# Optimization experiments

Hardware: AMD Instinct MI355X
Metric: run time of the kernel (lower is better)

The kernel has to match this reference:

```python
import jax, jax.numpy as jnp
import numpy as np

B, L, D, C, H, NB = 2, 2048, 256, 8, 8, 2
S = 2                        # spatial coord dim of s
E = 2 * D - (C + 1)          # id-embedding width per D*2-(C+1)
FIN = 1 + S + E + C          # z + s + id-embed + conditionals
MAXLOC = 4096
DH = (2 * D) // H            # per-head dim


def _ln(x, sc, b):
    m = x.mean(-1, keepdims=True)
    v = ((x - m) ** 2).mean(-1, keepdims=True)
    return (x - m) * jax.lax.rsqrt(v + 1e-6) * sc + b


def setup_inputs() -> dict:
    key = jax.random.key(0)
    ks = iter(jax.random.split(key, 64))
    nrm = lambda shape: jax.random.normal(next(ks), shape, jnp.float32) * 0.02
    inp = {
        "z": jax.random.normal(next(ks), (B, L), jnp.float32),
        "conditionals": jax.random.normal(next(ks), (C,), jnp.float32),
        "s": jax.random.uniform(next(ks), (L, S), jnp.float32),
        "K": jax.random.uniform(next(ks), (L, L), jnp.float32),
        "embed": nrm((MAXLOC, E)),
        "W_in1": nrm((FIN, 4 * D)), "b_in1": jnp.zeros((4 * D,), jnp.float32),
        "W_in2": nrm((4 * D, D)), "b_in2": jnp.zeros((D,), jnp.float32),
        "bias_w": jnp.ones((NB,), jnp.float32), "bias_b": jnp.zeros((NB,), jnp.float32),
        "Wq": nrm((NB, D, 2 * D)), "bq": jnp.zeros((NB, 2 * D), jnp.float32),
        "Wk": nrm((NB, D, 2 * D)), "bk": jnp.zeros((NB, 2 * D), jnp.float32),
        "Wv": nrm((NB, D, 2 * D)), "bv": jnp.zeros((NB, 2 * D), jnp.float32),
        "Wo": nrm((NB, 2 * D, D)), "bo": jnp.zeros((NB, D), jnp.float32),
        "ln1_s": jnp.ones((NB, D), jnp.float32), "ln1_b": jnp.zeros((NB, D), jnp.float32),
        "ln2_s": jnp.ones((NB, D), jnp.float32), "ln2_b": jnp.zeros((NB, D), jnp.float32),
        "Wf1": nrm((NB, D, 4 * D)), "bf1": jnp.zeros((NB, 4 * D), jnp.float32),
        "Wf2": nrm((NB, 4 * D, D)), "bf2": jnp.zeros((NB, D), jnp.float32),
        "Wh1": nrm((D, 128)), "bh1": jnp.zeros((128,), jnp.float32),
        "Wh2": nrm((128, 1)), "bh2": jnp.zeros((1,), jnp.float32),
    }
    return inp


def reference(z, conditionals, s, K, embed, W_in1, b_in1, W_in2, b_in2,
              bias_w, bias_b, Wq, bq, Wk, bk, Wv, bv, Wo, bo,
              ln1_s, ln1_b, ln2_s, ln2_b, Wf1, bf1, Wf2, bf2,
              Wh1, bh1, Wh2, bh2):
    Bx, Lx = z.shape
    ids_e = embed[:Lx]  # ids = arange(L), so embedding lookup is a leading slice
    feats = jnp.concatenate([
        z[..., None],                                          # (B, L, 1)
        jnp.broadcast_to(s[None], (Bx, Lx, S)),                # (B, L, S)
        jnp.broadcast_to(ids_e[None], (Bx, Lx, E)),            # (B, L, E)
        jnp.broadcast_to(conditionals[None, None], (Bx, Lx, C)),  # cond_as_feats
    ], axis=-1)
    x = jax.nn.gelu(feats @ W_in1 + b_in1) @ W_in2 + b_in2     # (B, L, D)
    for i in range(NB):
        bias = bias_w[i] * K + bias_b[i]                        # learned scalar-affine kernel bias (L, L)
        h = _ln(x, ln1_s[i], ln1_b[i])
        q = (h @ Wq[i] + bq[i]).reshape(Bx, Lx, H, DH)
        k = (h @ Wk[i] + bk[i]).reshape(Bx, Lx, H, DH)
        v = (h @ Wv[i] + bv[i]).reshape(Bx, Lx, H, DH)
        scores = jnp.einsum('bqhd,bkhd->bhqk', q, k) / jnp.sqrt(jnp.float32(DH))
        scores = scores + bias[None, None]                      # broadcast over batch, heads
        a = jax.nn.softmax(scores, axis=-1)
        o = jnp.einsum('bhqk,bkhd->bqhd', a, v).reshape(Bx, Lx, 2 * D)
        x = x + (o @ Wo[i] + bo[i])
        h2 = _ln(x, ln2_s[i], ln2_b[i])
        x = x + jax.nn.gelu(h2 @ Wf1[i] + bf1[i]) @ Wf2[i] + bf2[i]
    return jax.nn.gelu(x @ Wh1 + bh1) @ Wh2 + bh2              # head MLP([128,1]) -> (B, L, 1)
```

## Files before the change

kernel.cpp:

```cpp
#include <hip/hip_runtime.h>
#include <math.h>

#define B_SZ 2
#define L_LEN 2048
#define D_MOD 256
#define H_HEADS 8
#define NB_BLK 2
#define S_SZ 2
#define E_SZ 503
#define C_SZ 8
#define FIN 514
#define FIN_PAD 576
#define LOG2E 1.44269504088896340736f
#define QSC (0.125f * LOG2E)

typedef short bf16x8 __attribute__((ext_vector_type(8)));
typedef float f32x4 __attribute__((ext_vector_type(4)));
typedef unsigned short u16x4 __attribute__((ext_vector_type(4)));
typedef unsigned short u16x8 __attribute__((ext_vector_type(8)));

#define OFF_IN1 0
#define OFF_IN2 589824
#define OFF_QKV 851968
#define OFF_O   1638400
#define OFF_F1  1900544
#define OFF_F2  2424832
#define OFF_H   2949120
#define WT_END  2981888

__device__ __forceinline__ unsigned short f2bf(float x) {
    unsigned u = __float_as_uint(x);
    u += 0x7FFFu + ((u >> 16) & 1u);
    return (unsigned short)(u >> 16);
}

__device__ __forceinline__ float gelu_f(float x) {
    float x3 = x * x * x;
    return 0.5f * x * (1.0f + tanhf(0.7978845608028654f * (x + 0.044715f * x3)));
}

__device__ __forceinline__ void gll16(const void* g, void* l) {
    __builtin_amdgcn_global_load_lds(
        (const __attribute__((address_space(1))) unsigned int*)g,
        (__attribute__((address_space(3))) unsigned int*)l,
        16, 0, 0);
}

__global__ __launch_bounds__(256) void feats_kernel(
    const float* __restrict__ z, const float* __restrict__ s,
    const float* __restrict__ embed, const float* __restrict__ cond,
    unsigned short* __restrict__ feats)
{
    int idx = blockIdx.x * 256 + threadIdx.x;
    const int total = B_SZ * L_LEN * FIN_PAD;
    if (idx >= total) return;
    int f = idx % FIN_PAD;
    int row = idx / FIN_PAD;
    int l = row % L_LEN;
    float val;
    if (f == 0)                   val = z[row];
    else if (f < 1 + S_SZ)        val = s[l * S_SZ + (f - 1)];
    else if (f < 1 + S_SZ + E_SZ) val = embed[(size_t)l * E_SZ + (f - 3)];
    else if (f < FIN)             val = cond[f - (1 + S_SZ + E_SZ)];
    else                          val = 0.0f;
    feats[idx] = f2bf(val);
}

__global__ __launch_bounds__(256) void wprep_kernel(
    const float* __restrict__ W_in1, const float* __restrict__ W_in2,
    const float* __restrict__ Wq, const float* __restrict__ Wk,
    const float* __restrict__ Wv, const float* __restrict__ Wo,
    const float* __restrict__ Wf1, const float* __restrict__ Wf2,
    const float* __restrict__ Wh1, unsigned short* __restrict__ wt)
{
    int b = blockIdx.x;
    const float* src; unsigned short* dst; int K, N, Kp, tile;
    float scale = 1.0f;
    if (b < 144)      { src = W_in1; dst = wt + OFF_IN1; K = 514;  N = 1024; Kp = 576;  tile = b; }
    else if (b < 208) { src = W_in2; dst = wt + OFF_IN2; K = 1024; N = 256;  Kp = 1024; tile = b - 144; }
    else if (b < 400) { int t2 = b - 208;
                        int sec = t2 >> 5; tile = t2 & 31;
                        int i = sec / 3, which = sec % 3;
                        const float* wsrc = which == 0 ? Wq : which == 1 ? Wk : Wv;
                        if (which == 0) scale = QSC;
                        src = wsrc + (size_t)i * 131072;
                        dst = wt + OFF_QKV + (size_t)i * 393216 + (size_t)which * 131072;
                        K = 256; N = 512; Kp = 256; }
    else if (b < 464) { int t2 = b - 400; int i = t2 >> 5; tile = t2 & 31;
                        src = Wo + (size_t)i * 131072; dst = wt + OFF_O + (size_t)i * 131072;
                        K = 512; N = 256; Kp = 512; }
    else if (b < 592) { int t2 = b - 464; int i = t2 >> 6; tile = t2 & 63;
                        src = Wf1 + (size_t)i * 262144; dst = wt + OFF_F1 + (size_t)i * 262144;
                        K = 256; N = 1024; Kp = 256; }
    else if (b < 720) { int t2 = b - 592; int i = t2 >> 6; tile = t2 & 63;
                        src = Wf2 + (size_t)i * 262144; dst = wt + OFF_F2 + (size_t)i * 262144;
                        K = 1024; N = 256; Kp = 1024; }
    else              { tile = b - 720; src = Wh1; dst = wt + OFF_H;
                        K = 256; N = 128; Kp = 256; }

    int nt = N >> 6;
    int kt0 = (tile / nt) << 6;
    int nt0 = (tile % nt) << 6;

    __shared__ unsigned short sT[64][65];
    int t = threadIdx.x;
    #pragma unroll
    for (int p = 0; p < 4; p++) {
        int r = p * 16 + (t >> 4);
        int c = (t & 15) * 4;
        float4 v4 = make_float4(0.f, 0.f, 0.f, 0.f);
        if (kt0 + r < K) v4 = *(const float4*)(src + (size_t)(kt0 + r) * N + nt0 + c);
        sT[r][c + 0] = f2bf(v4.x * scale);
        sT[r][c + 1] = f2bf(v4.y * scale);
        sT[r][c + 2] = f2bf(v4.z * scale);
        sT[r][c + 3] = f2bf(v4.w * scale);
    }
    __syncthreads();
    int n = t >> 2, kq = (t & 3) * 16;
    u16x8 o0, o1;
    #pragma unroll
    for (int j = 0; j < 8; j++) {
        o0[j] = sT[kq + j][n];
        o1[j] = sT[kq + 8 + j][n];
    }
    unsigned short* dp = dst + (size_t)(nt0 + n) * Kp + kt0 + kq;
    *(u16x8*)(dp) = o0;
    *(u16x8*)(dp + 8) = o1;
}

__global__ __launch_bounds__(256) void kprep_kernel(
    const float* __restrict__ Kmat, const float* __restrict__ bias_w,
    unsigned short* __restrict__ kbt)
{
    __shared__ float sT[64][65];
    int tile = blockIdx.x;
    int qt0 = (tile & 31) << 6, kt0 = (tile >> 5) << 6;
    int t = threadIdx.x;
    int rr = t >> 4, cc = (t & 15) << 2;
    #pragma unroll
    for (int p = 0; p < 4; p++) {
        int qr = p * 16 + rr;
        float4 v4 = *(const float4*)(Kmat + (size_t)(qt0 + qr) * L_LEN + kt0 + cc);
        sT[cc + 0][qr] = v4.x;
        sT[cc + 1][qr] = v4.y;
        sT[cc + 2][qr] = v4.z;
        sT[cc + 3][qr] = v4.w;
    }
    __syncthreads();
    float s0 = bias_w[0] * LOG2E, s1 = bias_w[1] * LOG2E;
    int kr = t >> 2, qc = (t & 3) << 4;
    u16x8 a0, a1, b0, b1;
    #pragma unroll
    for (int j = 0; j < 8; j++) {
        float v = sT[kr][qc + j];
        a0[j] = f2bf(v * s0); b0[j] = f2bf(v * s1);
        float v2 = sT[kr][qc + 8 + j];
        a1[j] = f2bf(v2 * s0); b1[j] = f2bf(v2 * s1);
    }
    unsigned short* d0 = kbt + (size_t)(kt0 + kr) * L_LEN + qt0 + qc;
    *(u16x8*)d0 = a0; *(u16x8*)(d0 + 8) = a1;
    unsigned short* d1 = d0 + (size_t)L_LEN * L_LEN;
    *(u16x8*)d1 = b0; *(u16x8*)(d1 + 8) = b1;
}

__global__ __launch_bounds__(256) void bprep_kernel(
    const float* __restrict__ bq, const float* __restrict__ bk,
    const float* __restrict__ bv, float* __restrict__ bqkv)
{
    int idx = blockIdx.x * 256 + threadIdx.x;
    if (idx >= 2 * 1536) return;
    int i = idx / 1536, c = idx % 1536;
    float v;
    if (c < 512)       v = bq[i * 512 + c] * QSC;
    else if (c < 1024) v = bk[i * 512 + c - 512];
    else               v = bv[i * 512 + c - 1024];
    bqkv[idx] = v;
}

__global__ __launch_bounds__(256) void cvt_kernel(
    const float* __restrict__ x, unsigned short* __restrict__ xb)
{
    int idx = (blockIdx.x * 256 + threadIdx.x) * 8;
    float4 a = *(const float4*)(x + idx);
    float4 b = *(const float4*)(x + idx + 4);
    u16x8 o = { f2bf(a.x), f2bf(a.y), f2bf(a.z), f2bf(a.w),
                f2bf(b.x), f2bf(b.y), f2bf(b.z), f2bf(b.w) };
    *(u16x8*)(xb + idx) = o;
}

template<int ACT, int OMODE, int BM>
__global__ __launch_bounds__(256) void gemm_bf16(
    const unsigned short* __restrict__ A, const unsigned short* __restrict__ Wt,
    const float* __restrict__ bias, float* __restrict__ Cf,
    unsigned short* __restrict__ Cb, unsigned short* __restrict__ Cbk,
    unsigned short* __restrict__ Cbv, int M, int N, int Kd, int lda)
{
    __shared__ unsigned short sA[2][BM][64];
    __shared__ unsigned short sB[2][64][64];
    const int tid = threadIdx.x;
    const int l = tid & 63, w = tid >> 6;
    const int g = l >> 4, n16 = l & 15;
    const int m0 = blockIdx.y * BM, n0 = blockIdx.x * 64;

    const int r8 = l >> 3;
    const int swz8 = ((l & 7) ^ r8) * 8;

    const int NMI = (BM == 64) ? 2 : 1;
    const int wr = (BM == 64) ? (w >> 1) : (w >> 1);
    const int wc = w & 1;

    f32x4 acc[2][2];
    #pragma unroll
    for (int mi = 0; mi < 2; mi++)
        #pragma unroll
        for (int ni = 0; ni < 2; ni++)
            acc[mi][ni] = (f32x4){0.f, 0.f, 0.f, 0.f};

#define STAGE(buf, k0)                                                          \
    do {                                                                        \
        if (BM == 64) {                                                         \
            _Pragma("unroll")                                                   \
            for (int p = 0; p < 2; p++) {                                       \
                int row = w * 16 + p * 8 + r8;                                  \
                gll16(A + (size_t)(m0 + row) * lda + (k0) + swz8,               \
                      &sA[buf][w * 16 + p * 8][0]);                             \
            }                                                                   \
        } else {                                                                \
            int row = w * 8 + r8;                                               \
            gll16(A + (size_t)(m0 + row) * lda + (k0) + swz8,                   \
                  &sA[buf][w * 8][0]);                                          \
        }                                                                       \
        _Pragma("unroll")                                                       \
        for (int p = 0; p < 2; p++) {                                           \
            int row = w * 16 + p * 8 + r8;                                      \
            gll16(Wt + (size_t)(n0 + row) * Kd + (k0) + swz8,                   \
                  &sB[buf][w * 16 + p * 8][0]);                                 \
        }                                                                       \
    } while (0)

    STAGE(0, 0);
    __syncthreads();

    int cur = 0;
    for (int k0 = 0; k0 < Kd; k0 += 64) {
        int nxt = cur ^ 1;
        if (k0 + 64 < Kd) STAGE(nxt, k0 + 64);
        #pragma unroll
        for (int ks = 0; ks < 2; ks++) {
            bf16x8 af[2], bfr[2];
            #pragma unroll
            for (int mi = 0; mi < NMI; mi++) {
                int row = (BM == 64) ? (wr * 32 + mi * 16 + n16) : (wr * 16 + n16);
                af[mi] = *(const bf16x8*)((const char*)&sA[cur][row][0]
                          + ((ks * 64 + g * 16) ^ ((n16 & 7) << 4)));
            }
            #pragma unroll
            for (int ni = 0; ni < 2; ni++) {
                int row = wc * 32 + ni * 16 + n16;
                bfr[ni] = *(const bf16x8*)((const char*)&sB[cur][row][0]
                          + ((ks * 64 + g * 16) ^ ((n16 & 7) << 4)));
            }
            #pragma unroll
            for (int mi = 0; mi < NMI; mi++)
                #pragma unroll
                for (int ni = 0; ni < 2; ni++)
                    acc[mi][ni] = __builtin_amdgcn_mfma_f32_16x16x32_bf16(
                        af[mi], bfr[ni], acc[mi][ni], 0, 0, 0);
        }
        __syncthreads();
        cur = nxt;
    }
#undef STAGE

    #pragma unroll
    for (int mi = 0; mi < NMI; mi++) {
        #pragma unroll
        for (int ni = 0; ni < 2; ni++) {
            int col = n0 + wc * 32 + ni * 16 + n16;
            float bv = bias[col];
            #pragma unroll
            for (int r = 0; r < 4; r++) {
                int row = (BM == 64) ? (m0 + wr * 32 + mi * 16 + 4 * g + r)
                                     : (m0 + wr * 16 + 4 * g + r);
                float val = acc[mi][ni][r] + bv;
                if (ACT == 1) val = gelu_f(val);
                if (OMODE == 0) {
                    Cf[(size_t)row * N + col] = val;
                } else if (OMODE == 1) {
                    Cb[(size_t)row * N + col] = f2bf(val);
                } else if (OMODE == 2) {
                    float* cp = Cf + (size_t)row * N + col;
                    *cp += val;
                } else {
                    if (col < 1024) {
                        unsigned short* dst = (col < 512) ? Cb : Cbk;
                        dst[(size_t)row * 512 + (col & 511)] = f2bf(val);
                    } else {
                        Cbv[((size_t)(row >> 11) * 512 + (col - 1024)) * L_LEN + (row & (L_LEN - 1))] = f2bf(val);
                    }
                }
            }
        }
    }
}

__global__ __launch_bounds__(256) void ln_bf16(
    const float* __restrict__ x, const float* __restrict__ sc,
    const float* __restrict__ bi, unsigned short* __restrict__ out)
{
    int wave = threadIdx.x >> 6, lane = threadIdx.x & 63;
    int row = blockIdx.x * 4 + wave;
    const float* xr = x + (size_t)row * D_MOD;
    float4 v = *(const float4*)(xr + lane * 4);
    float s1 = v.x + v.y + v.z + v.w;
    float s2 = v.x * v.x + v.y * v.y + v.z * v.z + v.w * v.w;
    #pragma unroll
    for (int off = 1; off < 64; off <<= 1) {
        s1 += __shfl_xor(s1, off);
        s2 += __shfl_xor(s2, off);
    }
    float mean = s1 * (1.0f / 256.0f);
    float var = s2 * (1.0f / 256.0f) - mean * mean;
    float rs = rsqrtf(var + 1e-6f);
    float4 scv = *(const float4*)(sc + lane * 4);
    float4 bv  = *(const float4*)(bi + lane * 4);
    u16x4 o4;
    o4[0] = f2bf((v.x - mean) * rs * scv.x + bv.x);
    o4[1] = f2bf((v.y - mean) * rs * scv.y + bv.y);
    o4[2] = f2bf((v.z - mean) * rs * scv.z + bv.z);
    o4[3] = f2bf((v.w - mean) * rs * scv.w + bv.w);
    *(u16x4*)(out + (size_t)row * D_MOD + lane * 4) = o4;
}

__global__ __launch_bounds__(256, 3) void attn_mfma(
    const unsigned short* __restrict__ q, const unsigned short* __restrict__ k,
    const unsigned short* __restrict__ vt, const unsigned short* __restrict__ kmt,
    unsigned short* __restrict__ o)
{
    __shared__ unsigned short sK[2][64][64];
    __shared__ unsigned short sV[2][64][64];
    __shared__ unsigned short sKmT[64][64];
    __shared__ unsigned short sP[4][16][72];

    const int tid = threadIdx.x;
    const int l = tid & 63, w = tid >> 6;
    const int g = l >> 4, n16 = l & 15;
    const int qblk = blockIdx.x * 64, hh = blockIdx.y, b = blockIdx.z;

    const int r8 = l >> 3;
    const int swz8 = ((l & 7) ^ r8) * 8;

    bf16x8 qf[2];
    {
        const unsigned short* qp = q + (size_t)(b * L_LEN + qblk + w * 16 + n16) * 512 + hh * 64;
        qf[0] = *(const bf16x8*)(qp + g * 8);
        qf[1] = *(const bf16x8*)(qp + 32 + g * 8);
    }
    bf16x8 onesf;
    #pragma unroll
    for (int j = 0; j < 8; j++) onesf[j] = (short)0x3F80;

    f32x4 o_acc[4];
    #pragma unroll
    for (int c = 0; c < 4; c++) o_acc[c] = (f32x4){0.f, 0.f, 0.f, 0.f};
    f32x4 l_acc = (f32x4){0.f, 0.f, 0.f, 0.f};

    const unsigned short* kbase = k + (size_t)b * L_LEN * 512 + hh * 64;
    const unsigned short* vbase = vt + ((size_t)b * 512 + hh * 64) * L_LEN;

    #pragma unroll
    for (int p = 0; p < 2; p++) {
        int row = w * 16 + p * 8 + r8;
        gll16(kbase + (size_t)row * 512 + swz8, &sK[0][w * 16 + p * 8][0]);
        gll16(vbase + (size_t)row * L_LEN + swz8, &sV[0][w * 16 + p * 8][0]);
        gll16(kmt + (size_t)row * L_LEN + qblk + swz8, &sKmT[w * 16 + p * 8][0]);
    }
    __syncthreads();

    int cur = 0;
    for (int kt = 0; kt < L_LEN / 64; kt++) {
        const int nb = cur ^ 1;
        const int kblk2 = (kt + 1) << 6;
        if (kt + 1 < L_LEN / 64) {
            #pragma unroll
            for (int p = 0; p < 2; p++) {
                int row = w * 16 + p * 8 + r8;
                gll16(kbase + (size_t)(kblk2 + row) * 512 + swz8, &sK[nb][w * 16 + p * 8][0]);
                gll16(vbase + (size_t)row * L_LEN + kblk2 + swz8, &sV[nb][w * 16 + p * 8][0]);
            }
        }
        f32x4 sacc[4];
        #pragma unroll
        for (int c = 0; c < 4; c++) {
            const char* kb_ = (const char*)&sKmT[c * 16 + n16][0];
            u16x4 kmv = *(const u16x4*)(kb_ + ((32 * w + 8 * g) ^ ((n16 & 7) << 4)));
            #pragma unroll
            for (int r = 0; r < 4; r++)
                sacc[c][r] = __uint_as_float(((unsigned)(unsigned short)kmv[r]) << 16);
        }
        #pragma unroll
        for (int ks = 0; ks < 2; ks++)
            #pragma unroll
            for (int c = 0; c < 4; c++) {
                int row = c * 16 + n16;
                bf16x8 kf = *(const bf16x8*)((const char*)&sK[cur][row][0]
                             + ((ks * 64 + g * 16) ^ ((n16 & 7) << 4)));
                sacc[c] = __builtin_amdgcn_mfma_f32_16x16x32_bf16(qf[ks], kf, sacc[c], 0, 0, 0);
            }
        float p[4][4];
        #pragma unroll
        for (int r = 0; r < 4; r++)
            #pragma unroll
            for (int c = 0; c < 4; c++)
                p[r][c] = __builtin_amdgcn_exp2f(sacc[c][r]);
        asm volatile("s_waitcnt lgkmcnt(0)" ::: "memory");
        __builtin_amdgcn_s_barrier();
        __builtin_amdgcn_sched_barrier(0);
        if (kt + 1 < L_LEN / 64) {
            #pragma unroll
            for (int p2 = 0; p2 < 2; p2++) {
                int row = w * 16 + p2 * 8 + r8;
                gll16(kmt + (size_t)(kblk2 + row) * L_LEN + qblk + swz8,
                      &sKmT[w * 16 + p2 * 8][0]);
            }
        }
        #pragma unroll
        for (int r = 0; r < 4; r++)
            #pragma unroll
            for (int c = 0; c < 4; c++)
                sP[w][4 * g + r][c * 16 + n16] = f2bf(p[r][c]);
        #pragma unroll
        for (int ks = 0; ks < 2; ks++) {
            bf16x8 pf = *(const bf16x8*)&sP[w][n16][ks * 32 + g * 8];
            l_acc = __builtin_amdgcn_mfma_f32_16x16x32_bf16(pf, onesf, l_acc, 0, 0, 0);
            #pragma unroll
            for (int c = 0; c < 4; c++) {
                int row = c * 16 + n16;
                bf16x8 vf = *(const bf16x8*)((const char*)&sV[cur][row][0]
                             + ((ks * 64 + g * 16) ^ ((n16 & 7) << 4)));
                o_acc[c] = __builtin_amdgcn_mfma_f32_16x16x32_bf16(pf, vf, o_acc[c], 0, 0, 0);
            }
        }
        __syncthreads();
        cur = nb;
    }

    float inv[4];
    #pragma unroll
    for (int r = 0; r < 4; r++) inv[r] = 1.0f / l_acc[r];
    #pragma unroll
    for (int c = 0; c < 4; c++)
        #pragma unroll
        for (int r = 0; r < 4; r++)
            o[(size_t)(b * L_LEN + qblk + w * 16 + 4 * g + r) * 512 + hh * 64 + c * 16 + n16]
                = f2bf(o_acc[c][r] * inv[r]);
}

__global__ __launch_bounds__(256) void hsum_kernel(
    const unsigned short* __restrict__ hb, const float* __restrict__ Wh2,
    const float* __restrict__ bh2, float* __restrict__ out)
{
    int wave = threadIdx.x >> 6, lane = threadIdx.x & 63;
    int row = blockIdx.x * 4 + wave;
    unsigned v = *(const unsigned*)(hb + (size_t)row * 128 + lane * 2);
    float v0 = __uint_as_float((v & 0xFFFFu) << 16);
    float v1 = __uint_as_float(v & 0xFFFF0000u);
    float val = v0 * Wh2[lane * 2] + v1 * Wh2[lane * 2 + 1];
    #pragma unroll
    for (int off = 1; off < 64; off <<= 1)
        val += __shfl_xor(val, off);
    if (lane == 0) out[row] = val + bh2[0];
}

extern "C" void kernel_launch(void* const* d_in, const int* in_sizes, int n_in,
                              void* d_out, int out_size, void* d_ws, size_t ws_size,
                              hipStream_t stream)
{
    const float* z      = (const float*)d_in[0];
    const float* cond   = (const float*)d_in[1];
    const float* s      = (const float*)d_in[2];
    const float* Kmat   = (const float*)d_in[3];
    const float* embed  = (const float*)d_in[4];
    const float* W_in1  = (const float*)d_in[5];
    const float* b_in1  = (const float*)d_in[6];
    const float* W_in2  = (const float*)d_in[7];
    const float* b_in2  = (const float*)d_in[8];
    const float* bias_w = (const float*)d_in[9];
    const float* bias_b = (const float*)d_in[10];
    const float* Wq     = (const float*)d_in[11];
    const float* bq     = (const float*)d_in[12];
    const float* Wk     = (const float*)d_in[13];
    const float* bk     = (const float*)d_in[14];
    const float* Wv     = (const float*)d_in[15];
    const float* bv     = (const float*)d_in[16];
    const float* Wo     = (const float*)d_in[17];
    const float* bo     = (const float*)d_in[18];
    const float* ln1_s  = (const float*)d_in[19];
    const float* ln1_b  = (const float*)d_in[20];
    const float* ln2_s  = (const float*)d_in[21];
    const float* ln2_b  = (const float*)d_in[22];
    const float* Wf1    = (const float*)d_in[23];
    const float* bf1    = (const float*)d_in[24];
    const float* Wf2    = (const float*)d_in[25];
    const float* bf2    = (const float*)d_in[26];
    const float* Wh1    = (const float*)d_in[27];
    const float* bh1    = (const float*)d_in[28];
    const float* Wh2    = (const float*)d_in[29];
    const float* bh2    = (const float*)d_in[30];
    float* out = (float*)d_out;
    (void)bias_b;

    const int M = B_SZ * L_LEN;
    char* base = (char*)d_ws;
    unsigned short* feats = (unsigned short*)base;
    float* x = (float*)(base + (size_t)M * FIN_PAD * 2);
    unsigned short* h    = (unsigned short*)((char*)x + (size_t)M * D_MOD * 4);
    unsigned short* hid1 = h    + (size_t)M * D_MOD;
    unsigned short* qb   = hid1 + (size_t)M * 1024;
    unsigned short* kb2  = qb   + (size_t)M * 512;
    unsigned short* vtb  = kb2  + (size_t)M * 512;
    unsigned short* ob   = vtb  + (size_t)M * 512;
    unsigned short* wt   = ob   + (size_t)M * 512;
    float* bqkv          = (float*)(wt + WT_END);
    unsigned short* kbt  = (unsigned short*)(bqkv + 2 * 1536);

    wprep_kernel<<<dim3(728), dim3(256), 0, stream>>>(W_in1, W_in2, Wq, Wk, Wv, Wo, Wf1, Wf2, Wh1, wt);
    kprep_kernel<<<dim3(1024), dim3(256), 0, stream>>>(Kmat, bias_w, kbt);
    bprep_kernel<<<dim3(12), dim3(256), 0, stream>>>(bq, bk, bv, bqkv);
    feats_kernel<<<dim3((M * FIN_PAD) / 256), dim3(256), 0, stream>>>(z, s, embed, cond, feats);

    gemm_bf16<1, 1, 64><<<dim3(16, 64), 256, 0, stream>>>(feats, wt + OFF_IN1, b_in1, nullptr, hid1, nullptr, nullptr, M, 1024, FIN_PAD, FIN_PAD);
    gemm_bf16<0, 0, 32><<<dim3(4, 128), 256, 0, stream>>>(hid1, wt + OFF_IN2, b_in2, x, nullptr, nullptr, nullptr, M, 256, 1024, 1024);

    for (int i = 0; i < NB_BLK; i++) {
        ln_bf16<<<dim3(M / 4), 256, 0, stream>>>(x, ln1_s + i * D_MOD, ln1_b + i * D_MOD, h);
        gemm_bf16<0, 4, 64><<<dim3(24, 64), 256, 0, stream>>>(h, wt + OFF_QKV + (size_t)i * 393216, bqkv + i * 1536, nullptr, qb, kb2, vtb, M, 1536, 256, 256);
        attn_mfma<<<dim3(L_LEN / 64, H_HEADS, B_SZ), 256, 0, stream>>>(qb, kb2, vtb, kbt + (size_t)i * L_LEN * L_LEN, ob);
        gemm_bf16<0, 2, 32><<<dim3(4, 128), 256, 0, stream>>>(ob, wt + OFF_O + (size_t)i * 131072, bo + i * D_MOD, x, nullptr, nullptr, nullptr, M, 256, 512, 512);
        ln_bf16<<<dim3(M / 4), 256, 0, stream>>>(x, ln2_s + i * D_MOD, ln2_b + i * D_MOD, h);
        gemm_bf16<1, 1, 64><<<dim3(16, 64), 256, 0, stream>>>(h, wt + OFF_F1 + (size_t)i * 262144, bf1 + i * 1024, nullptr, hid1, nullptr, nullptr, M, 1024, 256, 256);
        gemm_bf16<0, 2, 32><<<dim3(4, 128), 256, 0, stream>>>(hid1, wt + OFF_F2 + (size_t)i * 262144, bf2 + i * D_MOD, x, nullptr, nullptr, nullptr, M, 256, 1024, 1024);
    }
    cvt_kernel<<<dim3(512), dim3(256), 0, stream>>>(x, h);
    gemm_bf16<1, 1, 64><<<dim3(2, 64), 256, 0, stream>>>(h, wt + OFF_H, bh1, nullptr, qb, nullptr, nullptr, M, 128, 256, 256);
    hsum_kernel<<<dim3(M / 4), 256, 0, stream>>>(qb, Wh2, bh2, out);
}
```

Baseline: 258.0 us.

## Split attention over KV halves, load kernel bias into registers, split-bf16 head GEMM

```diff
diff --git a/kernel.cpp b/kernel.cpp
--- a/kernel.cpp
+++ b/kernel.cpp
@@ -26,12 +26,16 @@
 #define OFF_F1  1900544
 #define OFF_F2  2424832
 #define OFF_H   2949120
-#define WT_END  2981888
+#define WT_END  3047424
 
 __device__ __forceinline__ unsigned short f2bf(float x) {
     unsigned u = __float_as_uint(x);
     u += 0x7FFFu + ((u >> 16) & 1u);
     return (unsigned short)(u >> 16);
+}
+
+__device__ __forceinline__ float bf2f(unsigned short h) {
+    return __uint_as_float(((unsigned)h) << 16);
 }
 
 __device__ __forceinline__ float gelu_f(float x) {
@@ -71,7 +75,7 @@
     const float* __restrict__ Wq, const float* __restrict__ Wk,
     const float* __restrict__ Wv, const float* __restrict__ Wo,
     const float* __restrict__ Wf1, const float* __restrict__ Wf2,
-    const float* __restrict__ Wh1, unsigned short* __restrict__ wt)
+    unsigned short* __restrict__ wt)
 {
     int b = blockIdx.x;
     const float* src; unsigned short* dst; int K, N, Kp, tile;
@@ -92,11 +96,9 @@
     else if (b < 592) { int t2 = b - 464; int i = t2 >> 6; tile = t2 & 63;
                         src = Wf1 + (size_t)i * 262144; dst = wt + OFF_F1 + (size_t)i * 262144;
                         K = 256; N = 1024; Kp = 256; }
-    else if (b < 720) { int t2 = b - 592; int i = t2 >> 6; tile = t2 & 63;
+    else              { int t2 = b - 592; int i = t2 >> 6; tile = t2 & 63;
                         src = Wf2 + (size_t)i * 262144; dst = wt + OFF_F2 + (size_t)i * 262144;
                         K = 1024; N = 256; Kp = 1024; }
-    else              { tile = b - 720; src = Wh1; dst = wt + OFF_H;
-                        K = 256; N = 128; Kp = 256; }
 
     int nt = N >> 6;
     int kt0 = (tile / nt) << 6;
@@ -128,6 +130,19 @@
     *(u16x8*)(dp + 8) = o1;
 }
 
+__global__ __launch_bounds__(256) void hprep_kernel(
+    const float* __restrict__ Wh1, unsigned short* __restrict__ whb)
+{
+    int idx = blockIdx.x * 256 + threadIdx.x;
+    if (idx >= 128 * 768) return;
+    int n = idx / 768, kk = idx % 768;
+    int kz = kk & 255;
+    float v = Wh1[(size_t)kz * 128 + n];
+    unsigned short hi = f2bf(v);
+    unsigned short res = (kk < 512) ? hi : f2bf(v - bf2f(hi));
+    whb[idx] = res;
+}
+
 __global__ __launch_bounds__(256) void kprep_kernel(
     const float* __restrict__ Kmat, const float* __restrict__ bias_w,
     unsigned short* __restrict__ kbt)
@@ -177,15 +192,24 @@
     bqkv[idx] = v;
 }
 
-__global__ __launch_bounds__(256) void cvt_kernel(
+__global__ __launch_bounds__(256) void xsplit_kernel(
     const float* __restrict__ x, unsigned short* __restrict__ xb)
 {
-    int idx = (blockIdx.x * 256 + threadIdx.x) * 8;
-    float4 a = *(const float4*)(x + idx);
-    float4 b = *(const float4*)(x + idx + 4);
-    u16x8 o = { f2bf(a.x), f2bf(a.y), f2bf(a.z), f2bf(a.w),
-                f2bf(b.x), f2bf(b.y), f2bf(b.z), f2bf(b.w) };
-    *(u16x8*)(xb + idx) = o;
+    int t = blockIdx.x * 256 + threadIdx.x;
+    int row = t >> 5, c8 = (t & 31) * 8;
+    const float* xr = x + (size_t)row * 256 + c8;
+    float4 a = *(const float4*)(xr);
+    float4 b4 = *(const float4*)(xr + 4);
+    u16x8 hi = { f2bf(a.x), f2bf(a.y), f2bf(a.z), f2bf(a.w),
+                 f2bf(b4.x), f2bf(b4.y), f2bf(b4.z), f2bf(b4.w) };
+    u16x8 lo = { f2bf(a.x - bf2f(hi[0])), f2bf(a.y - bf2f(hi[1])),
+                 f2bf(a.z - bf2f(hi[2])), f2bf(a.w - bf2f(hi[3])),
+                 f2bf(b4.x - bf2f(hi[4])), f2bf(b4.y - bf2f(hi[5])),
+                 f2bf(b4.z - bf2f(hi[6])), f2bf(b4.w - bf2f(hi[7])) };
+    unsigned short* orow = xb + (size_t)row * 768;
+    *(u16x8*)(orow + c8) = hi;
+    *(u16x8*)(orow + 256 + c8) = lo;
+    *(u16x8*)(orow + 512 + c8) = hi;
 }
 
 template<int ACT, int OMODE, int BM>
@@ -206,7 +230,7 @@
     const int swz8 = ((l & 7) ^ r8) * 8;
 
     const int NMI = (BM == 64) ? 2 : 1;
-    const int wr = (BM == 64) ? (w >> 1) : (w >> 1);
+    const int wr = w >> 1;
     const int wc = w & 1;
 
     f32x4 acc[2][2];
@@ -335,17 +359,18 @@
 __global__ __launch_bounds__(256, 3) void attn_mfma(
     const unsigned short* __restrict__ q, const unsigned short* __restrict__ k,
     const unsigned short* __restrict__ vt, const unsigned short* __restrict__ kmt,
-    unsigned short* __restrict__ o)
+    float* __restrict__ po, float* __restrict__ pl)
 {
     __shared__ unsigned short sK[2][64][64];
     __shared__ unsigned short sV[2][64][64];
-    __shared__ unsigned short sKmT[64][64];
     __shared__ unsigned short sP[4][16][72];
 
     const int tid = threadIdx.x;
     const int l = tid & 63, w = tid >> 6;
     const int g = l >> 4, n16 = l & 15;
-    const int qblk = blockIdx.x * 64, hh = blockIdx.y, b = blockIdx.z;
+    const int qblk = blockIdx.x * 64, hh = blockIdx.y;
+    const int b = blockIdx.z >> 1, part = blockIdx.z & 1;
+    const int kv0 = part * 1024;
 
     const int r8 = l >> 3;
     const int swz8 = ((l & 7) ^ r8) * 8;
@@ -365,39 +390,45 @@
     for (int c = 0; c < 4; c++) o_acc[c] = (f32x4){0.f, 0.f, 0.f, 0.f};
     f32x4 l_acc = (f32x4){0.f, 0.f, 0.f, 0.f};
 
-    const unsigned short* kbase = k + (size_t)b * L_LEN * 512 + hh * 64;
-    const unsigned short* vbase = vt + ((size_t)b * 512 + hh * 64) * L_LEN;
+    const unsigned short* kbase = k + ((size_t)(b * L_LEN) + kv0) * 512 + hh * 64;
+    const unsigned short* vbase = vt + ((size_t)b * 512 + hh * 64) * L_LEN + kv0;
+    const unsigned short* kmbase = kmt + (size_t)kv0 * L_LEN + qblk + 16 * w + 4 * g;
+
+    u16x4 kmC[4], kmN[4];
 
     #pragma unroll
     for (int p = 0; p < 2; p++) {
         int row = w * 16 + p * 8 + r8;
         gll16(kbase + (size_t)row * 512 + swz8, &sK[0][w * 16 + p * 8][0]);
         gll16(vbase + (size_t)row * L_LEN + swz8, &sV[0][w * 16 + p * 8][0]);
-        gll16(kmt + (size_t)row * L_LEN + qblk + swz8, &sKmT[w * 16 + p * 8][0]);
-    }
+    }
+    #pragma unroll
+    for (int c = 0; c < 4; c++)
+        kmC[c] = *(const u16x4*)(kmbase + (size_t)(c * 16 + n16) * L_LEN);
     __syncthreads();
 
     int cur = 0;
-    for (int kt = 0; kt < L_LEN / 64; kt++) {
+    for (int kt = 0; kt < 16; kt++) {
         const int nb = cur ^ 1;
         const int kblk2 = (kt + 1) << 6;
-        if (kt + 1 < L_LEN / 64) {
+        if (kt + 1 < 16) {
             #pragma unroll
             for (int p = 0; p < 2; p++) {
                 int row = w * 16 + p * 8 + r8;
                 gll16(kbase + (size_t)(kblk2 + row) * 512 + swz8, &sK[nb][w * 16 + p * 8][0]);
                 gll16(vbase + (size_t)row * L_LEN + kblk2 + swz8, &sV[nb][w * 16 + p * 8][0]);
             }
+            #pragma unroll
+            for (int c = 0; c < 4; c++)
+                kmN[c] = *(const u16x4*)(kmbase + (size_t)(kblk2 + c * 16 + n16) * L_LEN);
         }
         f32x4 sacc[4];
         #pragma unroll
-        for (int c = 0; c < 4; c++) {
-            const char* kb_ = (const char*)&sKmT[c * 16 + n16][0];
-            u16x4 kmv = *(const u16x4*)(kb_ + ((32 * w + 8 * g) ^ ((n16 & 7) << 4)));
+        for (int c = 0; c < 4; c++)
             #pragma unroll
             for (int r = 0; r < 4; r++)
-                sacc[c][r] = __uint_as_float(((unsigned)(unsigned short)kmv[r]) << 16);
-        }
+                sacc[c][r] = bf2f((unsigned short)kmC[c][r]);
+        __builtin_amdgcn_s_setprio(1);
         #pragma unroll
         for (int ks = 0; ks < 2; ks++)
             #pragma unroll
@@ -407,28 +438,19 @@
                              + ((ks * 64 + g * 16) ^ ((n16 & 7) << 4)));
                 sacc[c] = __builtin_amdgcn_mfma_f32_16x16x32_bf16(qf[ks], kf, sacc[c], 0, 0, 0);
             }
+        __builtin_amdgcn_s_setprio(0);
         float p[4][4];
         #pragma unroll
         for (int r = 0; r < 4; r++)
             #pragma unroll
             for (int c = 0; c < 4; c++)
                 p[r][c] = __builtin_amdgcn_exp2f(sacc[c][r]);
-        asm volatile("s_waitcnt lgkmcnt(0)" ::: "memory");
-        __builtin_amdgcn_s_barrier();
-        __builtin_amdgcn_sched_barrier(0);
-        if (kt + 1 < L_LEN / 64) {
-            #pragma unroll
-            for (int p2 = 0; p2 < 2; p2++) {
-                int row = w * 16 + p2 * 8 + r8;
-                gll16(kmt + (size_t)(kblk2 + row) * L_LEN + qblk + swz8,
-                      &sKmT[w * 16 + p2 * 8][0]);
-            }
-        }
         #pragma unroll
         for (int r = 0; r < 4; r++)
             #pragma unroll
             for (int c = 0; c < 4; c++)
                 sP[w][4 * g + r][c * 16 + n16] = f2bf(p[r][c]);
+        __builtin_amdgcn_s_setprio(1);
         #pragma unroll
         for (int ks = 0; ks < 2; ks++) {
             bf16x8 pf = *(const bf16x8*)&sP[w][n16][ks * 32 + g * 8];
@@ -441,19 +463,42 @@
                 o_acc[c] = __builtin_amdgcn_mfma_f32_16x16x32_bf16(pf, vf, o_acc[c], 0, 0, 0);
             }
         }
+        __builtin_amdgcn_s_setprio(0);
         __syncthreads();
         cur = nb;
-    }
-
-    float inv[4];
-    #pragma unroll
-    for (int r = 0; r < 4; r++) inv[r] = 1.0f / l_acc[r];
+        #pragma unroll
+        for (int c = 0; c < 4; c++) kmC[c] = kmN[c];
+    }
+
+    float* pob = po + (size_t)part * 4096 * 512;
     #pragma unroll
     for (int c = 0; c < 4; c++)
         #pragma unroll
         for (int r = 0; r < 4; r++)
-            o[(size_t)(b * L_LEN + qblk + w * 16 + 4 * g + r) * 512 + hh * 64 + c * 16 + n16]
-                = f2bf(o_acc[c][r] * inv[r]);
+            pob[(size_t)(b * L_LEN + qblk + w * 16 + 4 * g + r) * 512 + hh * 64 + c * 16 + n16]
+                = o_acc[c][r];
+    if (n16 == 0) {
+        #pragma unroll
+        for (int r = 0; r < 4; r++)
+            pl[(size_t)part * 32768 + (size_t)(b * L_LEN + qblk + w * 16 + 4 * g + r) * 8 + hh]
+                = l_acc[r];
+    }
+}
+
+__global__ __launch_bounds__(256) void attn_combine(
+    const float* __restrict__ po, const float* __restrict__ pl,
+    unsigned short* __restrict__ ob)
+{
+    int idx = (blockIdx.x * 256 + threadIdx.x) * 4;
+    int row = idx >> 9, col = idx & 511, hh = col >> 6;
+    float4 a = *(const float4*)(po + idx);
+    float4 b4 = *(const float4*)(po + (size_t)4096 * 512 + idx);
+    float l0 = pl[(size_t)row * 8 + hh];
+    float l1 = pl[32768 + (size_t)row * 8 + hh];
+    float inv = 1.0f / (l0 + l1);
+    u16x4 o = { f2bf((a.x + b4.x) * inv), f2bf((a.y + b4.y) * inv),
+                f2bf((a.z + b4.z) * inv), f2bf((a.w + b4.w) * inv) };
+    *(u16x4*)(ob + idx) = o;
 }
 
 __global__ __launch_bounds__(256) void hsum_kernel(
@@ -523,8 +568,11 @@
     unsigned short* wt   = ob   + (size_t)M * 512;
     float* bqkv          = (float*)(wt + WT_END);
     unsigned short* kbt  = (unsigned short*)(bqkv + 2 * 1536);
-
-    wprep_kernel<<<dim3(728), dim3(256), 0, stream>>>(W_in1, W_in2, Wq, Wk, Wv, Wo, Wf1, Wf2, Wh1, wt);
+    float* po            = (float*)(kbt + (size_t)2 * L_LEN * L_LEN);
+    float* pl            = po + (size_t)2 * 4096 * 512;
+
+    wprep_kernel<<<dim3(720), dim3(256), 0, stream>>>(W_in1, W_in2, Wq, Wk, Wv, Wo, Wf1, Wf2, wt);
+    hprep_kernel<<<dim3(384), dim3(256), 0, stream>>>(Wh1, wt + OFF_H);
     kprep_kernel<<<dim3(1024), dim3(256), 0, stream>>>(Kmat, bias_w, kbt);
     bprep_kernel<<<dim3(12), dim3(256), 0, stream>>>(bq, bk, bv, bqkv);
     feats_kernel<<<dim3((M * FIN_PAD) / 256), dim3(256), 0, stream>>>(z, s, embed, cond, feats);
@@ -535,13 +583,14 @@
     for (int i = 0; i < NB_BLK; i++) {
         ln_bf16<<<dim3(M / 4), 256, 0, stream>>>(x, ln1_s + i * D_MOD, ln1_b + i * D_MOD, h);
         gemm_bf16<0, 4, 64><<<dim3(24, 64), 256, 0, stream>>>(h, wt + OFF_QKV + (size_t)i * 393216, bqkv + i * 1536, nullptr, qb, kb2, vtb, M, 1536, 256, 256);
-        attn_mfma<<<dim3(L_LEN / 64, H_HEADS, B_SZ), 256, 0, stream>>>(qb, kb2, vtb, kbt + (size_t)i * L_LEN * L_LEN, ob);
+        attn_mfma<<<dim3(L_LEN / 64, H_HEADS, 2 * B_SZ), 256, 0, stream>>>(qb, kb2, vtb, kbt + (size_t)i * L_LEN * L_LEN, po, pl);
+        attn_combine<<<dim3(2048), 256, 0, stream>>>(po, pl, ob);
         gemm_bf16<0, 2, 32><<<dim3(4, 128), 256, 0, stream>>>(ob, wt + OFF_O + (size_t)i * 131072, bo + i * D_MOD, x, nullptr, nullptr, nullptr, M, 256, 512, 512);
         ln_bf16<<<dim3(M / 4), 256, 0, stream>>>(x, ln2_s + i * D_MOD, ln2_b + i * D_MOD, h);
         gemm_bf16<1, 1, 64><<<dim3(16, 64), 256, 0, stream>>>(h, wt + OFF_F1 + (size_t)i * 262144, bf1 + i * 1024, nullptr, hid1, nullptr, nullptr, M, 1024, 256, 256);
         gemm_bf16<0, 2, 32><<<dim3(4, 128), 256, 0, stream>>>(hid1, wt + OFF_F2 + (size_t)i * 262144, bf2 + i * D_MOD, x, nullptr, nullptr, nullptr, M, 256, 1024, 1024);
     }
-    cvt_kernel<<<dim3(512), dim3(256), 0, stream>>>(x, h);
-    gemm_bf16<1, 1, 64><<<dim3(2, 64), 256, 0, stream>>>(h, wt + OFF_H, bh1, nullptr, qb, nullptr, nullptr, M, 128, 256, 256);
+    xsplit_kernel<<<dim3(512), dim3(256), 0, stream>>>(x, hid1);
+    gemm_bf16<1, 1, 64><<<dim3(2, 64), 256, 0, stream>>>(hid1, wt + OFF_H, bh1, nullptr, qb, nullptr, nullptr, M, 128, 768, 768);
     hsum_kernel<<<dim3(M / 4), 256, 0, stream>>>(qb, Wh2, bh2, out);
 }
```

Result: slower. 292.7 us (+13.5%).

## Add 128x128 GEMM tile for wide projections, split-bf16 head GEMM, attention setprio

Applied to the files above, without the earlier changes.

```diff
diff --git a/kernel.cpp b/kernel.cpp
--- a/kernel.cpp
+++ b/kernel.cpp
@@ -26,12 +26,16 @@
 #define OFF_F1  1900544
 #define OFF_F2  2424832
 #define OFF_H   2949120
-#define WT_END  2981888
+#define WT_END  3047424
 
 __device__ __forceinline__ unsigned short f2bf(float x) {
     unsigned u = __float_as_uint(x);
     u += 0x7FFFu + ((u >> 16) & 1u);
     return (unsigned short)(u >> 16);
+}
+
+__device__ __forceinline__ float bf2f(unsigned short h) {
+    return __uint_as_float(((unsigned)h) << 16);
 }
 
 __device__ __forceinline__ float gelu_f(float x) {
@@ -71,7 +75,7 @@
     const float* __restrict__ Wq, const float* __restrict__ Wk,
     const float* __restrict__ Wv, const float* __restrict__ Wo,
     const float* __restrict__ Wf1, const float* __restrict__ Wf2,
-    const float* __restrict__ Wh1, unsigned short* __restrict__ wt)
+    unsigned short* __restrict__ wt)
 {
     int b = blockIdx.x;
     const float* src; unsigned short* dst; int K, N, Kp, tile;
@@ -92,11 +96,9 @@
     else if (b < 592) { int t2 = b - 464; int i = t2 >> 6; tile = t2 & 63;
                         src = Wf1 + (size_t)i * 262144; dst = wt + OFF_F1 + (size_t)i * 262144;
                         K = 256; N = 1024; Kp = 256; }
-    else if (b < 720) { int t2 = b - 592; int i = t2 >> 6; tile = t2 & 63;
+    else              { int t2 = b - 592; int i = t2 >> 6; tile = t2 & 63;
                         src = Wf2 + (size_t)i * 262144; dst = wt + OFF_F2 + (size_t)i * 262144;
                         K = 1024; N = 256; Kp = 1024; }
-    else              { tile = b - 720; src = Wh1; dst = wt + OFF_H;
-                        K = 256; N = 128; Kp = 256; }
 
     int nt = N >> 6;
     int kt0 = (tile / nt) << 6;
@@ -128,6 +130,19 @@
     *(u16x8*)(dp + 8) = o1;
 }
 
+__global__ __launch_bounds__(256) void hprep_kernel(
+    const float* __restrict__ Wh1, unsigned short* __restrict__ whb)
+{
+    int idx = blockIdx.x * 256 + threadIdx.x;
+    if (idx >= 128 * 768) return;
+    int n = idx / 768, kk = idx % 768;
+    int kz = kk & 255;
+    float v = Wh1[(size_t)kz * 128 + n];
+    unsigned short hi = f2bf(v);
+    unsigned short res = (kk < 512) ? hi : f2bf(v - bf2f(hi));
+    whb[idx] = res;
+}
+
 __global__ __launch_bounds__(256) void kprep_kernel(
     const float* __restrict__ Kmat, const float* __restrict__ bias_w,
     unsigned short* __restrict__ kbt)
@@ -177,23 +192,114 @@
     bqkv[idx] = v;
 }
 
-__global__ __launch_bounds__(256) void cvt_kernel(
+__global__ __launch_bounds__(256) void xsplit_kernel(
     const float* __restrict__ x, unsigned short* __restrict__ xb)
 {
-    int idx = (blockIdx.x * 256 + threadIdx.x) * 8;
-    float4 a = *(const float4*)(x + idx);
-    float4 b = *(const float4*)(x + idx + 4);
-    u16x8 o = { f2bf(a.x), f2bf(a.y), f2bf(a.z), f2bf(a.w),
-                f2bf(b.x), f2bf(b.y), f2bf(b.z), f2bf(b.w) };
-    *(u16x8*)(xb + idx) = o;
+    int t = blockIdx.x * 256 + threadIdx.x;
+    int row = t >> 5, c8 = (t & 31) * 8;
+    const float* xr = x + (size_t)row * 256 + c8;
+    float4 a = *(const float4*)(xr);
+    float4 b4 = *(const float4*)(xr + 4);
+    u16x8 hi = { f2bf(a.x), f2bf(a.y), f2bf(a.z), f2bf(a.w),
+                 f2bf(b4.x), f2bf(b4.y), f2bf(b4.z), f2bf(b4.w) };
+    u16x8 lo = { f2bf(a.x - bf2f(hi[0])), f2bf(a.y - bf2f(hi[1])),
+                 f2bf(a.z - bf2f(hi[2])), f2bf(a.w - bf2f(hi[3])),
+                 f2bf(b4.x - bf2f(hi[4])), f2bf(b4.y - bf2f(hi[5])),
+                 f2bf(b4.z - bf2f(hi[6])), f2bf(b4.w - bf2f(hi[7])) };
+    unsigned short* orow = xb + (size_t)row * 768;
+    *(u16x8*)(orow + c8) = hi;
+    *(u16x8*)(orow + 256 + c8) = lo;
+    *(u16x8*)(orow + 512 + c8) = hi;
+}
+
+template<int ACT, int OMODE>
+__global__ __launch_bounds__(256) void gemm128(
+    const unsigned short* __restrict__ A, const unsigned short* __restrict__ Wt,
+    const float* __restrict__ bias, unsigned short* __restrict__ Cb,
+    unsigned short* __restrict__ Cbk, unsigned short* __restrict__ Cbv,
+    int M, int N, int Kd, int lda)
+{
+    __shared__ unsigned short sA[128][64];
+    __shared__ unsigned short sB[128][64];
+    const int tid = threadIdx.x;
+    const int l = tid & 63, w = tid >> 6;
+    const int g = l >> 4, n16 = l & 15;
+    const int wr = w >> 1, wc = w & 1;
+    const int m0 = blockIdx.y * 128, n0 = blockIdx.x * 128;
+    const int r8 = l >> 3;
+    const int swz8 = ((l & 7) ^ r8) * 8;
+
+    f32x4 acc[4][4];
+    #pragma unroll
+    for (int mi = 0; mi < 4; mi++)
+        #pragma unroll
+        for (int ni = 0; ni < 4; ni++)
+            acc[mi][ni] = (f32x4){0.f, 0.f, 0.f, 0.f};
+
+    for (int k0 = 0; k0 < Kd; k0 += 64) {
+        if (k0) __syncthreads();
+        #pragma unroll
+        for (int p = 0; p < 4; p++) {
+            int row = w * 32 + p * 8 + r8;
+            gll16(A  + (size_t)(m0 + row) * lda + k0 + swz8, &sA[w * 32 + p * 8][0]);
+            gll16(Wt + (size_t)(n0 + row) * Kd  + k0 + swz8, &sB[w * 32 + p * 8][0]);
+        }
+        __syncthreads();
+        #pragma unroll
+        for (int ks = 0; ks < 2; ks++) {
+            bf16x8 af[4], bfr[4];
+            #pragma unroll
+            for (int mi = 0; mi < 4; mi++) {
+                int row = wr * 64 + mi * 16 + n16;
+                af[mi] = *(const bf16x8*)((const char*)&sA[row][0]
+                          + ((ks * 64 + g * 16) ^ ((n16 & 7) << 4)));
+            }
+            #pragma unroll
+            for (int ni = 0; ni < 4; ni++) {
+                int row = wc * 64 + ni * 16 + n16;
+                bfr[ni] = *(const bf16x8*)((const char*)&sB[row][0]
+                          + ((ks * 64 + g * 16) ^ ((n16 & 7) << 4)));
+            }
+            #pragma unroll
+            for (int mi = 0; mi < 4; mi++)
+                #pragma unroll
+                for (int ni = 0; ni < 4; ni++)
+                    acc[mi][ni] = __builtin_amdgcn_mfma_f32_16x16x32_bf16(
+                        af[mi], bfr[ni], acc[mi][ni], 0, 0, 0);
+        }
+    }
+
+    #pragma unroll
+    for (int mi = 0; mi < 4; mi++) {
+        #pragma unroll
+        for (int ni = 0; ni < 4; ni++) {
+            int col = n0 + wc * 64 + ni * 16 + n16;
+            float bv = bias[col];
+            #pragma unroll
+            for (int r = 0; r < 4; r++) {
+                int row = m0 + wr * 64 + mi * 16 + 4 * g + r;
+                float val = acc[mi][ni][r] + bv;
+                if (ACT == 1) val = gelu_f(val);
+                if (OMODE == 1) {
+                    Cb[(size_t)row * N + col] = f2bf(val);
+                } else {
+                    if (col < 1024) {
+                        unsigned short* dst = (col < 512) ? Cb : Cbk;
+                        dst[(size_t)row * 512 + (col & 511)] = f2bf(val);
+                    } else {
+                        Cbv[((size_t)(row >> 11) * 512 + (col - 1024)) * L_LEN + (row & (L_LEN - 1))] = f2bf(val);
+                    }
+                }
+            }
+        }
+    }
 }
 
 template<int ACT, int OMODE, int BM>
 __global__ __launch_bounds__(256) void gemm_bf16(
     const unsigned short* __restrict__ A, const unsigned short* __restrict__ Wt,
     const float* __restrict__ bias, float* __restrict__ Cf,
-    unsigned short* __restrict__ Cb, unsigned short* __restrict__ Cbk,
-    unsigned short* __restrict__ Cbv, int M, int N, int Kd, int lda)
+    unsigned short* __restrict__ Cb, int M, int N, int Kd, int lda)
 {
     __shared__ unsigned short sA[2][BM][64];
     __shared__ unsigned short sB[2][64][64];
@@ -206,7 +312,7 @@
     const int swz8 = ((l & 7) ^ r8) * 8;
 
     const int NMI = (BM == 64) ? 2 : 1;
-    const int wr = (BM == 64) ? (w >> 1) : (w >> 1);
+    const int wr = w >> 1;
     const int wc = w & 1;
 
     f32x4 acc[2][2];
@@ -288,16 +394,9 @@
                     Cf[(size_t)row * N + col] = val;
                 } else if (OMODE == 1) {
                     Cb[(size_t)row * N + col] = f2bf(val);
-                } else if (OMODE == 2) {
+                } else {
                     float* cp = Cf + (size_t)row * N + col;
                     *cp += val;
-                } else {
-                    if (col < 1024) {
-                        unsigned short* dst = (col < 512) ? Cb : Cbk;
-                        dst[(size_t)row * 512 + (col & 511)] = f2bf(val);
-                    } else {
-                        Cbv[((size_t)(row >> 11) * 512 + (col - 1024)) * L_LEN + (row & (L_LEN - 1))] = f2bf(val);
-                    }
                 }
             }
         }
@@ -396,8 +495,9 @@
             u16x4 kmv = *(const u16x4*)(kb_ + ((32 * w + 8 * g) ^ ((n16 & 7) << 4)));
             #pragma unroll
             for (int r = 0; r < 4; r++)
-                sacc[c][r] = __uint_as_float(((unsigned)(unsigned short)kmv[r]) << 16);
-        }
+                sacc[c][r] = bf2f((unsigned short)kmv[r]);
+        }
+        __builtin_amdgcn_s_setprio(1);
         #pragma unroll
         for (int ks = 0; ks < 2; ks++)
             #pragma unroll
@@ -407,6 +507,7 @@
                              + ((ks * 64 + g * 16) ^ ((n16 & 7) << 4)));
                 sacc[c] = __builtin_amdgcn_mfma_f32_16x16x32_bf16(qf[ks], kf, sacc[c], 0, 0, 0);
             }
+        __builtin_amdgcn_s_setprio(0);
         float p[4][4];
         #pragma unroll
         for (int r = 0; r < 4; r++)
@@ -429,6 +530,7 @@
             #pragma unroll
             for (int c = 0; c < 4; c++)
                 sP[w][4 * g + r][c * 16 + n16] = f2bf(p[r][c]);
+        __builtin_amdgcn_s_setprio(1);
         #pragma unroll
         for (int ks = 0; ks < 2; ks++) {
             bf16x8 pf = *(const bf16x8*)&sP[w][n16][ks * 32 + g * 8];
@@ -441,6 +543,7 @@
                 o_acc[c] = __builtin_amdgcn_mfma_f32_16x16x32_bf16(pf, vf, o_acc[c], 0, 0, 0);
             }
         }
+        __builtin_amdgcn_s_setprio(0);
         __syncthreads();
         cur = nb;
     }
@@ -524,24 +627,25 @@
     float* bqkv          = (float*)(wt + WT_END);
     unsigned short* kbt  = (unsigned short*)(bqkv + 2 * 1536);
 
-    wprep_kernel<<<dim3(728), dim3(256), 0, stream>>>(W_in1, W_in2, Wq, Wk, Wv, Wo, Wf1, Wf2, Wh1, wt);
+    wprep_kernel<<<dim3(720), dim3(256), 0, stream>>>(W_in1, W_in2, Wq, Wk, Wv, Wo, Wf1, Wf2, wt);
+    hprep_kernel<<<dim3(384), dim3(256), 0, stream>>>(Wh1, wt + OFF_H);
     kprep_kernel<<<dim3(1024), dim3(256), 0, stream>>>(Kmat, bias_w, kbt);
     bprep_kernel<<<dim3(12), dim3(256), 0, stream>>>(bq, bk, bv, bqkv);
     feats_kernel<<<dim3((M * FIN_PAD) / 256), dim3(256), 0, stream>>>(z, s, embed, cond, feats);
 
-    gemm_bf16<1, 1, 64><<<dim3(16, 64), 256, 0, stream>>>(feats, wt + OFF_IN1, b_in1, nullptr, hid1, nullptr, nullptr, M, 1024, FIN_PAD, FIN_PAD);
-    gemm_bf16<0, 0, 32><<<dim3(4, 128), 256, 0, stream>>>(hid1, wt + OFF_IN2, b_in2, x, nullptr, nullptr, nullptr, M, 256, 1024, 1024);
+    gemm128<1, 1><<<dim3(8, 32), 256, 0, stream>>>(feats, wt + OFF_IN1, b_in1, hid1, nullptr, nullptr, M, 1024, FIN_PAD, FIN_PAD);
+    gemm_bf16<0, 0, 32><<<dim3(4, 128), 256, 0, stream>>>(hid1, wt + OFF_IN2, b_in2, x, nullptr, M, 256, 1024, 1024);
 
     for (int i = 0; i < NB_BLK; i++) {
         ln_bf16<<<dim3(M / 4), 256, 0, stream>>>(x, ln1_s + i * D_MOD, ln1_b + i * D_MOD, h);
-        gemm_bf16<0, 4, 64><<<dim3(24, 64), 256, 0, stream>>>(h, wt + OFF_QKV + (size_t)i * 393216, bqkv + i * 1536, nullptr, qb, kb2, vtb, M, 1536, 256, 256);
+        gemm128<0, 4><<<dim3(12, 32), 256, 0, stream>>>(h, wt + OFF_QKV + (size_t)i * 393216, bqkv + i * 1536, qb, kb2, vtb, M, 1536, 256, 256);
         attn_mfma<<<dim3(L_LEN / 64, H_HEADS, B_SZ), 256, 0, stream>>>(qb, kb2, vtb, kbt + (size_t)i * L_LEN * L_LEN, ob);
-        gemm_bf16<0, 2, 32><<<dim3(4, 128), 256, 0, stream>>>(ob, wt + OFF_O + (size_t)i * 131072, bo + i * D_MOD, x, nullptr, nullptr, nullptr, M, 256, 512, 512);
+        gemm_bf16<0, 2, 32><<<dim3(4, 128), 256, 0, stream>>>(ob, wt + OFF_O + (size_t)i * 131072, bo + i * D_MOD, x, nullptr, M, 256, 512, 512);
         ln_bf16<<<dim3(M / 4), 256, 0, stream>>>(x, ln2_s + i * D_MOD, ln2_b + i * D_MOD, h);
-        gemm_bf16<1, 1, 64><<<dim3(16, 64), 256, 0, stream>>>(h, wt + OFF_F1 + (size_t)i * 262144, bf1 + i * 1024, nullptr, hid1, nullptr, nullptr, M, 1024, 256, 256);
-        gemm_bf16<0, 2, 32><<<dim3(4, 128), 256, 0, stream>>>(hid1, wt + OFF_F2 + (size_t)i * 262144, bf2 + i * D_MOD, x, nullptr, nullptr, nullptr, M, 256, 1024, 1024);
-    }
-    cvt_kernel<<<dim3(512), dim3(256), 0, stream>>>(x, h);
-    gemm_bf16<1, 1, 64><<<dim3(2, 64), 256, 0, stream>>>(h, wt + OFF_H, bh1, nullptr, qb, nullptr, nullptr, M, 128, 256, 256);
+        gemm128<1, 1><<<dim3(8, 32), 256, 0, stream>>>(h, wt + OFF_F1 + (size_t)i * 262144, bf1 + i * 1024, hid1, nullptr, nullptr, M, 1024, 256, 256);
+        gemm_bf16<0, 2, 32><<<dim3(4, 128), 256, 0, stream>>>(hid1, wt + OFF_F2 + (size_t)i * 262144, bf2 + i * D_MOD, x, nullptr, M, 256, 1024, 1024);
+    }
+    xsplit_kernel<<<dim3(512), dim3(256), 0, stream>>>(x, hid1);
+    gemm_bf16<1, 1, 64><<<dim3(2, 64), 256, 0, stream>>>(hid1, wt + OFF_H, bh1, nullptr, qb, M, 128, 768, 768);
     hsum_kernel<<<dim3(M / 4), 256, 0, stream>>>(qb, Wh2, bh2, out);
 }
```

New measurement: 283.8 us. 10.0% more time.
